# Optimization experiments

Hardware: AMD Instinct MI355X
Metric: run time of the kernel (lower is better)

## Reference

```python
import jax, jax.numpy as jnp
import numpy as np

N = 1 << 20          # ray samples
POS_DIM = 32         # levels * feature_dim (hash_encoding is identity stub)
DENSITY_W = 64
COLOR_W = 64


def sh4_encoding(d):
    # Fourth-order (degree-4, 16-component) real spherical harmonics, vectorized.
    x, y, z = d[..., 0], d[..., 1], d[..., 2]
    xx, yy, zz = x * x, y * y, z * z
    c0 = jnp.full_like(x, 0.28209479177387814)
    comps = [
        c0,
        0.4886025119029199 * y,
        0.4886025119029199 * z,
        0.4886025119029199 * x,
        1.0925484305920792 * x * y,
        1.0925484305920792 * y * z,
        0.9461746957575601 * zz - 0.31539156525252,
        1.0925484305920792 * x * z,
        0.5462742152960396 * (xx - yy),
        0.5900435899266435 * y * (3 * xx - yy),
        2.890611442640554 * x * y * z,
        0.4570457994644658 * y * (5 * zz - 1),
        0.3731763325901154 * z * (5 * zz - 3),
        0.4570457994644658 * x * (5 * zz - 1),
        1.445305721320277 * z * (xx - yy),
        0.5900435899266435 * x * (xx - 3 * yy),
    ]
    return jnp.stack(comps, axis=-1)  # [..., 16]


def setup_inputs() -> dict:
    key = jax.random.key(0)
    ks = jax.random.split(key, 8)
    def dense_init(k, fan_in, fan_out):
        # flax default: lecun_normal kernel, zeros bias
        w = jax.random.normal(k, (fan_in, fan_out), dtype=jnp.float32) / np.sqrt(fan_in)
        b = jnp.zeros((fan_out,), dtype=jnp.float32)
        return w, b
    position = jax.random.normal(ks[0], (N, POS_DIM), dtype=jnp.float32)
    direction = jax.random.normal(ks[1], (N, 3), dtype=jnp.float32)
    W1, b1 = dense_init(ks[2], POS_DIM, DENSITY_W)
    W2, b2 = dense_init(ks[3], DENSITY_W, 16)
    W3, b3 = dense_init(ks[4], 16 + 16, COLOR_W)
    W4, b4 = dense_init(ks[5], COLOR_W, COLOR_W)
    W5, b5 = dense_init(ks[6], COLOR_W, 3)
    return {
        "position": position, "direction": direction,
        "W1": W1, "b1": b1, "W2": W2, "b2": b2,
        "W3": W3, "b3": b3, "W4": W4, "b4": b4,
        "W5": W5, "b5": b5,
    }


def reference(position, direction, W1, b1, W2, b2, W3, b3, W4, b4, W5, b5):
    # Density MLP
    h = jax.nn.relu(position @ W1 + b1)        # [N, 64]
    density = h @ W2 + b2                      # [N, 16]
    # Color MLP on concat(density_feat, SH(dir))
    enc_dir = sh4_encoding(direction)          # [N, 16]
    c = jnp.concatenate([density, enc_dir], axis=-1)  # [N, 32]
    c = jax.nn.relu(c @ W3 + b3)               # [N, 64]
    c = jax.nn.relu(c @ W4 + b4)               # [N, 64]
    c = c @ W5 + b5                            # [N, 3]
    color = jax.nn.sigmoid(c)                  # high_dynamic_range=False
    return (density, color)
```

## Files before the change

### kernel.cpp

```cpp
#include <hip/hip_runtime.h>
#include <hip/hip_bf16.h>

typedef __bf16 bf16_t;
typedef __bf16 bf16x8 __attribute__((ext_vector_type(8)));
typedef float  f32x4  __attribute__((ext_vector_type(4)));

#define TPW   8
#define WAVES 4
#define ROWS_PER_BLOCK (WAVES * TPW * 16)
#define HS 68
#define CS 36

#define FENCE() __asm__ volatile("" ::: "memory")

__device__ __forceinline__ bf16x8 ldrow8(const float* base, size_t elem_off) {
    const float* p = base + elem_off;
    f32x4 a = *(const f32x4*)p;
    f32x4 b = *(const f32x4*)(p + 4);
    bf16x8 r;
    #pragma unroll
    for (int j = 0; j < 4; ++j) { r[j] = (bf16_t)a[j]; r[j+4] = (bf16_t)b[j]; }
    return r;
}

__global__ __launch_bounds__(256) void nerf_fused(
    const float* __restrict__ pos, const float* __restrict__ dir,
    const float* __restrict__ W1, const float* __restrict__ b1,
    const float* __restrict__ W2, const float* __restrict__ b2,
    const float* __restrict__ W3, const float* __restrict__ b3,
    const float* __restrict__ W4, const float* __restrict__ b4,
    const float* __restrict__ W5, const float* __restrict__ b5,
    float* __restrict__ outD, float* __restrict__ outC)
{
    __shared__ float hbuf[WAVES][16 * HS];
    __shared__ float cbuf[WAVES][16 * CS];

    const int tid  = threadIdx.x;
    const int w    = tid >> 6;
    const int lane = tid & 63;
    const int q    = lane >> 4;
    const int n    = lane & 15;

    float* hb = hbuf[w];
    float* cb = cbuf[w];

    bf16x8 w1f[4], w2f[2], w3f[4], w4f[2][4], w5f[2];
    #pragma unroll
    for (int t = 0; t < 4; ++t)
        #pragma unroll
        for (int j = 0; j < 8; ++j)
            w1f[t][j] = (bf16_t)W1[(8*q + j) * 64 + 16*t + n];
    #pragma unroll
    for (int kt = 0; kt < 2; ++kt)
        #pragma unroll
        for (int j = 0; j < 8; ++j)
            w2f[kt][j] = (bf16_t)W2[(32*kt + 8*q + j) * 16 + n];
    #pragma unroll
    for (int t = 0; t < 4; ++t)
        #pragma unroll
        for (int j = 0; j < 8; ++j)
            w3f[t][j] = (bf16_t)W3[(8*q + j) * 64 + 16*t + n];
    #pragma unroll
    for (int kt = 0; kt < 2; ++kt)
        #pragma unroll
        for (int t = 0; t < 4; ++t)
            #pragma unroll
            for (int j = 0; j < 8; ++j)
                w4f[kt][t][j] = (bf16_t)W4[(32*kt + 8*q + j) * 64 + 16*t + n];
    #pragma unroll
    for (int kt = 0; kt < 2; ++kt)
        #pragma unroll
        for (int j = 0; j < 8; ++j)
            w5f[kt][j] = (n < 3) ? (bf16_t)W5[(32*kt + 8*q + j) * 3 + n]
                                 : (bf16_t)0.0f;
    float b1f[4], b3f[4], b4f[4];
    #pragma unroll
    for (int t = 0; t < 4; ++t) {
        b1f[t] = b1[16*t + n];
        b3f[t] = b3[16*t + n];
        b4f[t] = b4[16*t + n];
    }
    const float b2f = b2[n];
    const float b5f = (n < 3) ? b5[n] : 0.0f;

    const f32x4 zero4 = {0.f, 0.f, 0.f, 0.f};

    const int waveRow0 = blockIdx.x * ROWS_PER_BLOCK + w * (TPW * 16);

    bf16x8 pfrag = ldrow8(pos, (size_t)(waveRow0 + n) * 32 + 8*q);

    for (int t = 0; t < TPW; ++t) {
        const int row0 = waveRow0 + t * 16;
        const int tn   = (t + 1 < TPW) ? t + 1 : t;
        bf16x8 pnext = ldrow8(pos, (size_t)(waveRow0 + tn*16 + n) * 32 + 8*q);

        f32x4 acc1[4];
        #pragma unroll
        for (int tt = 0; tt < 4; ++tt)
            acc1[tt] = __builtin_amdgcn_mfma_f32_16x16x32_bf16(pfrag, w1f[tt], zero4, 0, 0, 0);
        #pragma unroll
        for (int r = 0; r < 4; ++r) {
            float* p = hb + (4*q + r) * HS + n;
            p[0]  = fmaxf(acc1[0][r] + b1f[0], 0.f);
            p[16] = fmaxf(acc1[1][r] + b1f[1], 0.f);
            p[32] = fmaxf(acc1[2][r] + b1f[2], 0.f);
            p[48] = fmaxf(acc1[3][r] + b1f[3], 0.f);
        }
        FENCE();
        bf16x8 a2[2];
        #pragma unroll
        for (int kt = 0; kt < 2; ++kt) {
            const f32x4* pr = (const f32x4*)(hb + n * HS + 32*kt + 8*q);
            f32x4 u0 = pr[0], u1 = pr[1];
            #pragma unroll
            for (int j = 0; j < 4; ++j) { a2[kt][j] = (bf16_t)u0[j]; a2[kt][4+j] = (bf16_t)u1[j]; }
        }

        f32x4 acc2 = __builtin_amdgcn_mfma_f32_16x16x32_bf16(a2[0], w2f[0], zero4, 0, 0, 0);
        acc2 = __builtin_amdgcn_mfma_f32_16x16x32_bf16(a2[1], w2f[1], acc2, 0, 0, 0);
        {
            float* p = cb + (4*q) * CS + n;
            p[0]    = acc2[0] + b2f;
            p[CS]   = acc2[1] + b2f;
            p[2*CS] = acc2[2] + b2f;
            p[3*CS] = acc2[3] + b2f;
        }
        FENCE();

        {
            const int rr = lane >> 2;
            const int cg = lane & 3;
            f32x4 dv = *(const f32x4*)(cb + rr * CS + 4*cg);
            *(f32x4*)(outD + (size_t)(row0 + rr) * 16 + 4*cg) = dv;
        }

        float av[8];
        {
            const f32x4* pr = (const f32x4*)(cb + n * CS + 8*(q & 1));
            f32x4 u0 = pr[0], u1 = pr[1];
            #pragma unroll
            for (int j = 0; j < 4; ++j) { av[j] = u0[j]; av[4+j] = u1[j]; }
        }
        if (q >= 2) {
            const size_t db = (size_t)(row0 + n) * 3;
            const float x = dir[db + 0], y = dir[db + 1], z = dir[db + 2];
            const float xx = x*x, yy = y*y, zz = z*z;
            if (q == 2) {
                av[0] = 0.28209479177387814f;
                av[1] = 0.4886025119029199f * y;
                av[2] = 0.4886025119029199f * z;
                av[3] = 0.4886025119029199f * x;
                av[4] = 1.0925484305920792f * x * y;
                av[5] = 1.0925484305920792f * y * z;
                av[6] = 0.9461746957575601f * zz - 0.31539156525252f;
                av[7] = 1.0925484305920792f * x * z;
            } else {
                av[0] = 0.5462742152960396f * (xx - yy);
                av[1] = 0.5900435899266435f * y * (3.f*xx - yy);
                av[2] = 2.890611442640554f * x * y * z;
                av[3] = 0.4570457994644658f * y * (5.f*zz - 1.f);
                av[4] = 0.3731763325901154f * z * (5.f*zz - 3.f);
                av[5] = 0.4570457994644658f * x * (5.f*zz - 1.f);
                av[6] = 1.445305721320277f  * z * (xx - yy);
                av[7] = 0.5900435899266435f * x * (xx - 3.f*yy);
            }
        }
        bf16x8 a3;
        #pragma unroll
        for (int j = 0; j < 8; ++j) a3[j] = (bf16_t)av[j];

        f32x4 acc3[4];
        #pragma unroll
        for (int tt = 0; tt < 4; ++tt)
            acc3[tt] = __builtin_amdgcn_mfma_f32_16x16x32_bf16(a3, w3f[tt], zero4, 0, 0, 0);
        FENCE();
        #pragma unroll
        for (int r = 0; r < 4; ++r) {
            float* p = hb + (4*q + r) * HS + n;
            p[0]  = fmaxf(acc3[0][r] + b3f[0], 0.f);
            p[16] = fmaxf(acc3[1][r] + b3f[1], 0.f);
            p[32] = fmaxf(acc3[2][r] + b3f[2], 0.f);
            p[48] = fmaxf(acc3[3][r] + b3f[3], 0.f);
        }
        FENCE();
        bf16x8 a4[2];
        #pragma unroll
        for (int kt = 0; kt < 2; ++kt) {
            const f32x4* pr = (const f32x4*)(hb + n * HS + 32*kt + 8*q);
            f32x4 u0 = pr[0], u1 = pr[1];
            #pragma unroll
            for (int j = 0; j < 4; ++j) { a4[kt][j] = (bf16_t)u0[j]; a4[kt][4+j] = (bf16_t)u1[j]; }
        }

        f32x4 acc4[4];
        #pragma unroll
        for (int tt = 0; tt < 4; ++tt) {
            acc4[tt] = __builtin_amdgcn_mfma_f32_16x16x32_bf16(a4[0], w4f[0][tt], zero4, 0, 0, 0);
            acc4[tt] = __builtin_amdgcn_mfma_f32_16x16x32_bf16(a4[1], w4f[1][tt], acc4[tt], 0, 0, 0);
        }
        FENCE();
        #pragma unroll
        for (int r = 0; r < 4; ++r) {
            float* p = hb + (4*q + r) * HS + n;
            p[0]  = fmaxf(acc4[0][r] + b4f[0], 0.f);
            p[16] = fmaxf(acc4[1][r] + b4f[1], 0.f);
            p[32] = fmaxf(acc4[2][r] + b4f[2], 0.f);
            p[48] = fmaxf(acc4[3][r] + b4f[3], 0.f);
        }
        FENCE();
        bf16x8 a5[2];
        #pragma unroll
        for (int kt = 0; kt < 2; ++kt) {
            const f32x4* pr = (const f32x4*)(hb + n * HS + 32*kt + 8*q);
            f32x4 u0 = pr[0], u1 = pr[1];
            #pragma unroll
            for (int j = 0; j < 4; ++j) { a5[kt][j] = (bf16_t)u0[j]; a5[kt][4+j] = (bf16_t)u1[j]; }
        }

        f32x4 acc5 = __builtin_amdgcn_mfma_f32_16x16x32_bf16(a5[0], w5f[0], zero4, 0, 0, 0);
        acc5 = __builtin_amdgcn_mfma_f32_16x16x32_bf16(a5[1], w5f[1], acc5, 0, 0, 0);
        if (n < 3) {
            float* p = cb + (4*q) * CS + 32 + n;
            #pragma unroll
            for (int r = 0; r < 4; ++r) {
                float v = acc5[r] + b5f;
                p[r*CS] = 1.f / (1.f + __expf(-v));
            }
        }
        FENCE();
        if (lane < 48) {
            const int s = lane / 3, c = lane - 3*s;
            outC[(size_t)(row0 + s) * 3 + c] = cb[s * CS + 32 + c];
        }
        FENCE();

        pfrag = pnext;
    }
}

extern "C" void kernel_launch(void* const* d_in, const int* in_sizes, int n_in,
                              void* d_out, int out_size, void* d_ws, size_t ws_size,
                              hipStream_t stream) {
    const float* pos = (const float*)d_in[0];
    const float* dir = (const float*)d_in[1];
    const float* W1  = (const float*)d_in[2];
    const float* b1  = (const float*)d_in[3];
    const float* W2  = (const float*)d_in[4];
    const float* b2  = (const float*)d_in[5];
    const float* W3  = (const float*)d_in[6];
    const float* b3  = (const float*)d_in[7];
    const float* W4  = (const float*)d_in[8];
    const float* b4  = (const float*)d_in[9];
    const float* W5  = (const float*)d_in[10];
    const float* b5  = (const float*)d_in[11];

    const int N = in_sizes[0] / 32;
    float* outD = (float*)d_out;
    float* outC = outD + (size_t)N * 16;

    const int grid = N / ROWS_PER_BLOCK;
    nerf_fused<<<grid, WAVES * 64, 0, stream>>>(pos, dir, W1, b1, W2, b2, W3, b3,
                                                W4, b4, W5, b5, outD, outC);
}
```

Measured before the change: 283.7 us.

## Chain MLP layers in registers via transposed 16x16x16 MFMA, drop LDS hidden buffers

```diff
diff --git a/kernel.cpp b/kernel.cpp
--- a/kernel.cpp
+++ b/kernel.cpp
@@ -2,26 +2,29 @@
 #include <hip/hip_bf16.h>
 
 typedef __bf16 bf16_t;
-typedef __bf16 bf16x8 __attribute__((ext_vector_type(8)));
-typedef float  f32x4  __attribute__((ext_vector_type(4)));
+typedef short  s4    __attribute__((ext_vector_type(4)));
+typedef float  f32x4 __attribute__((ext_vector_type(4)));
 
 #define TPW   8
 #define WAVES 4
 #define ROWS_PER_BLOCK (WAVES * TPW * 16)
-#define HS 68
 #define CS 36
 
 #define FENCE() __asm__ volatile("" ::: "memory")
 
-__device__ __forceinline__ bf16x8 ldrow8(const float* base, size_t elem_off) {
-    const float* p = base + elem_off;
-    f32x4 a = *(const f32x4*)p;
-    f32x4 b = *(const f32x4*)(p + 4);
-    bf16x8 r;
-    #pragma unroll
-    for (int j = 0; j < 4; ++j) { r[j] = (bf16_t)a[j]; r[j+4] = (bf16_t)b[j]; }
+__device__ __forceinline__ short bfs(float f) {
+    return __builtin_bit_cast(short, (bf16_t)f);
+}
+__device__ __forceinline__ s4 pack4(f32x4 a) {
+    s4 r; r[0]=bfs(a[0]); r[1]=bfs(a[1]); r[2]=bfs(a[2]); r[3]=bfs(a[3]); return r;
+}
+__device__ __forceinline__ s4 relu_pack4(f32x4 a) {
+    s4 r;
+    r[0]=bfs(fmaxf(a[0],0.f)); r[1]=bfs(fmaxf(a[1],0.f));
+    r[2]=bfs(fmaxf(a[2],0.f)); r[3]=bfs(fmaxf(a[3],0.f));
     return r;
 }
+#define MFMA16(a,b,c) __builtin_amdgcn_mfma_f32_16x16x16bf16_1k(a, b, c, 0, 0, 0)
 
 __global__ __launch_bounds__(256) void nerf_fused(
     const float* __restrict__ pos, const float* __restrict__ dir,
@@ -32,7 +35,6 @@
     const float* __restrict__ W5, const float* __restrict__ b5,
     float* __restrict__ outD, float* __restrict__ outC)
 {
-    __shared__ float hbuf[WAVES][16 * HS];
     __shared__ float cbuf[WAVES][16 * CS];
 
     const int tid  = threadIdx.x;
@@ -41,92 +43,90 @@
     const int q    = lane >> 4;
     const int n    = lane & 15;
 
-    float* hb = hbuf[w];
     float* cb = cbuf[w];
 
-    bf16x8 w1f[4], w2f[2], w3f[4], w4f[2][4], w5f[2];
-    #pragma unroll
-    for (int t = 0; t < 4; ++t)
-        #pragma unroll
-        for (int j = 0; j < 8; ++j)
-            w1f[t][j] = (bf16_t)W1[(8*q + j) * 64 + 16*t + n];
-    #pragma unroll
-    for (int kt = 0; kt < 2; ++kt)
-        #pragma unroll
-        for (int j = 0; j < 8; ++j)
-            w2f[kt][j] = (bf16_t)W2[(32*kt + 8*q + j) * 16 + n];
-    #pragma unroll
-    for (int t = 0; t < 4; ++t)
-        #pragma unroll
-        for (int j = 0; j < 8; ++j)
-            w3f[t][j] = (bf16_t)W3[(8*q + j) * 64 + 16*t + n];
-    #pragma unroll
-    for (int kt = 0; kt < 2; ++kt)
-        #pragma unroll
-        for (int t = 0; t < 4; ++t)
-            #pragma unroll
-            for (int j = 0; j < 8; ++j)
-                w4f[kt][t][j] = (bf16_t)W4[(32*kt + 8*q + j) * 64 + 16*t + n];
-    #pragma unroll
-    for (int kt = 0; kt < 2; ++kt)
-        #pragma unroll
-        for (int j = 0; j < 8; ++j)
-            w5f[kt][j] = (n < 3) ? (bf16_t)W5[(32*kt + 8*q + j) * 3 + n]
-                                 : (bf16_t)0.0f;
-    float b1f[4], b3f[4], b4f[4];
-    #pragma unroll
-    for (int t = 0; t < 4; ++t) {
-        b1f[t] = b1[16*t + n];
-        b3f[t] = b3[16*t + n];
-        b4f[t] = b4[16*t + n];
+    s4 wa1[4][2], wa2[4], wa3[4][2], wa4[4][4], wa5[4];
+    #pragma unroll
+    for (int t = 0; t < 4; ++t)
+        #pragma unroll
+        for (int kt = 0; kt < 2; ++kt)
+            #pragma unroll
+            for (int i = 0; i < 4; ++i)
+                wa1[t][kt][i] = bfs(W1[(16*kt + 4*q + i) * 64 + 16*t + n]);
+    #pragma unroll
+    for (int kt = 0; kt < 4; ++kt)
+        #pragma unroll
+        for (int i = 0; i < 4; ++i)
+            wa2[kt][i] = bfs(W2[(16*kt + 4*q + i) * 16 + n]);
+    #pragma unroll
+    for (int t = 0; t < 4; ++t)
+        #pragma unroll
+        for (int kt = 0; kt < 2; ++kt)
+            #pragma unroll
+            for (int i = 0; i < 4; ++i)
+                wa3[t][kt][i] = bfs(W3[(16*kt + 4*q + i) * 64 + 16*t + n]);
+    #pragma unroll
+    for (int t = 0; t < 4; ++t)
+        #pragma unroll
+        for (int kt = 0; kt < 4; ++kt)
+            #pragma unroll
+            for (int i = 0; i < 4; ++i)
+                wa4[t][kt][i] = bfs(W4[(16*kt + 4*q + i) * 64 + 16*t + n]);
+    #pragma unroll
+    for (int kt = 0; kt < 4; ++kt)
+        #pragma unroll
+        for (int i = 0; i < 4; ++i)
+            wa5[kt][i] = (n < 3) ? bfs(W5[(16*kt + 4*q + i) * 3 + n]) : (short)0;
+
+    f32x4 bi1[4], bi3[4], bi4[4], bi2, bi5;
+    #pragma unroll
+    for (int t = 0; t < 4; ++t)
+        #pragma unroll
+        for (int r = 0; r < 4; ++r) {
+            bi1[t][r] = b1[16*t + 4*q + r];
+            bi3[t][r] = b3[16*t + 4*q + r];
+            bi4[t][r] = b4[16*t + 4*q + r];
+        }
+    #pragma unroll
+    for (int r = 0; r < 4; ++r) {
+        bi2[r] = b2[4*q + r];
+        bi5[r] = (q == 0 && r < 3) ? b5[r] : 0.f;
     }
-    const float b2f = b2[n];
-    const float b5f = (n < 3) ? b5[n] : 0.0f;
-
-    const f32x4 zero4 = {0.f, 0.f, 0.f, 0.f};
 
     const int waveRow0 = blockIdx.x * ROWS_PER_BLOCK + w * (TPW * 16);
 
-    bf16x8 pfrag = ldrow8(pos, (size_t)(waveRow0 + n) * 32 + 8*q);
+    f32x4 pa = *(const f32x4*)(pos + (size_t)(waveRow0 + n) * 32 + 4*q);
+    f32x4 pb = *(const f32x4*)(pos + (size_t)(waveRow0 + n) * 32 + 16 + 4*q);
+    float dx = dir[(size_t)(waveRow0 + n) * 3 + 0];
+    float dy = dir[(size_t)(waveRow0 + n) * 3 + 1];
+    float dz = dir[(size_t)(waveRow0 + n) * 3 + 2];
 
     for (int t = 0; t < TPW; ++t) {
         const int row0 = waveRow0 + t * 16;
-        const int tn   = (t + 1 < TPW) ? t + 1 : t;
-        bf16x8 pnext = ldrow8(pos, (size_t)(waveRow0 + tn*16 + n) * 32 + 8*q);
-
-        f32x4 acc1[4];
-        #pragma unroll
-        for (int tt = 0; tt < 4; ++tt)
-            acc1[tt] = __builtin_amdgcn_mfma_f32_16x16x32_bf16(pfrag, w1f[tt], zero4, 0, 0, 0);
-        #pragma unroll
-        for (int r = 0; r < 4; ++r) {
-            float* p = hb + (4*q + r) * HS + n;
-            p[0]  = fmaxf(acc1[0][r] + b1f[0], 0.f);
-            p[16] = fmaxf(acc1[1][r] + b1f[1], 0.f);
-            p[32] = fmaxf(acc1[2][r] + b1f[2], 0.f);
-            p[48] = fmaxf(acc1[3][r] + b1f[3], 0.f);
-        }
+        const int rn   = waveRow0 + ((t + 1 < TPW) ? t + 1 : t) * 16;
+        f32x4 pa2 = *(const f32x4*)(pos + (size_t)(rn + n) * 32 + 4*q);
+        f32x4 pb2 = *(const f32x4*)(pos + (size_t)(rn + n) * 32 + 16 + 4*q);
+        float dx2 = dir[(size_t)(rn + n) * 3 + 0];
+        float dy2 = dir[(size_t)(rn + n) * 3 + 1];
+        float dz2 = dir[(size_t)(rn + n) * 3 + 2];
+
+        s4 xb0 = pack4(pa), xb1 = pack4(pb);
+
+        s4 hf[4];
+        #pragma unroll
+        for (int tt = 0; tt < 4; ++tt) {
+            f32x4 h = MFMA16(wa1[tt][0], xb0, bi1[tt]);
+            h = MFMA16(wa1[tt][1], xb1, h);
+            hf[tt] = relu_pack4(h);
+        }
+
+        f32x4 d2 = bi2;
+        #pragma unroll
+        for (int kt = 0; kt < 4; ++kt)
+            d2 = MFMA16(wa2[kt], hf[kt], d2);
+
+        *(f32x4*)(cb + n * CS + 4*q) = d2;
         FENCE();
-        bf16x8 a2[2];
-        #pragma unroll
-        for (int kt = 0; kt < 2; ++kt) {
-            const f32x4* pr = (const f32x4*)(hb + n * HS + 32*kt + 8*q);
-            f32x4 u0 = pr[0], u1 = pr[1];
-            #pragma unroll
-            for (int j = 0; j < 4; ++j) { a2[kt][j] = (bf16_t)u0[j]; a2[kt][4+j] = (bf16_t)u1[j]; }
-        }
-
-        f32x4 acc2 = __builtin_amdgcn_mfma_f32_16x16x32_bf16(a2[0], w2f[0], zero4, 0, 0, 0);
-        acc2 = __builtin_amdgcn_mfma_f32_16x16x32_bf16(a2[1], w2f[1], acc2, 0, 0, 0);
-        {
-            float* p = cb + (4*q) * CS + n;
-            p[0]    = acc2[0] + b2f;
-            p[CS]   = acc2[1] + b2f;
-            p[2*CS] = acc2[2] + b2f;
-            p[3*CS] = acc2[3] + b2f;
-        }
-        FENCE();
-
         {
             const int rr = lane >> 2;
             const int cg = lane & 3;
@@ -134,98 +134,63 @@
             *(f32x4*)(outD + (size_t)(row0 + rr) * 16 + 4*cg) = dv;
         }
 
-        float av[8];
+        s4 cf0 = pack4(d2);
+        f32x4 shv;
         {
-            const f32x4* pr = (const f32x4*)(cb + n * CS + 8*(q & 1));
-            f32x4 u0 = pr[0], u1 = pr[1];
-            #pragma unroll
-            for (int j = 0; j < 4; ++j) { av[j] = u0[j]; av[4+j] = u1[j]; }
-        }
-        if (q >= 2) {
-            const size_t db = (size_t)(row0 + n) * 3;
-            const float x = dir[db + 0], y = dir[db + 1], z = dir[db + 2];
-            const float xx = x*x, yy = y*y, zz = z*z;
-            if (q == 2) {
-                av[0] = 0.28209479177387814f;
-                av[1] = 0.4886025119029199f * y;
-                av[2] = 0.4886025119029199f * z;
-                av[3] = 0.4886025119029199f * x;
-                av[4] = 1.0925484305920792f * x * y;
-                av[5] = 1.0925484305920792f * y * z;
-                av[6] = 0.9461746957575601f * zz - 0.31539156525252f;
-                av[7] = 1.0925484305920792f * x * z;
+            const float xx = dx*dx, yy = dy*dy, zz = dz*dz;
+            if (q == 0) {
+                shv[0] = 0.28209479177387814f;
+                shv[1] = 0.4886025119029199f * dy;
+                shv[2] = 0.4886025119029199f * dz;
+                shv[3] = 0.4886025119029199f * dx;
+            } else if (q == 1) {
+                shv[0] = 1.0925484305920792f * dx * dy;
+                shv[1] = 1.0925484305920792f * dy * dz;
+                shv[2] = 0.9461746957575601f * zz - 0.31539156525252f;
+                shv[3] = 1.0925484305920792f * dx * dz;
+            } else if (q == 2) {
+                shv[0] = 0.5462742152960396f * (xx - yy);
+                shv[1] = 0.5900435899266435f * dy * (3.f*xx - yy);
+                shv[2] = 2.890611442640554f * dx * dy * dz;
+                shv[3] = 0.4570457994644658f * dy * (5.f*zz - 1.f);
             } else {
-                av[0] = 0.5462742152960396f * (xx - yy);
-                av[1] = 0.5900435899266435f * y * (3.f*xx - yy);
-                av[2] = 2.890611442640554f * x * y * z;
-                av[3] = 0.4570457994644658f * y * (5.f*zz - 1.f);
-                av[4] = 0.3731763325901154f * z * (5.f*zz - 3.f);
-                av[5] = 0.4570457994644658f * x * (5.f*zz - 1.f);
-                av[6] = 1.445305721320277f  * z * (xx - yy);
-                av[7] = 0.5900435899266435f * x * (xx - 3.f*yy);
+                shv[0] = 0.3731763325901154f * dz * (5.f*zz - 3.f);
+                shv[1] = 0.4570457994644658f * dx * (5.f*zz - 1.f);
+                shv[2] = 1.445305721320277f  * dz * (xx - yy);
+                shv[3] = 0.5900435899266435f * dx * (xx - 3.f*yy);
             }
         }
-        bf16x8 a3;
-        #pragma unroll
-        for (int j = 0; j < 8; ++j) a3[j] = (bf16_t)av[j];
-
-        f32x4 acc3[4];
-        #pragma unroll
-        for (int tt = 0; tt < 4; ++tt)
-            acc3[tt] = __builtin_amdgcn_mfma_f32_16x16x32_bf16(a3, w3f[tt], zero4, 0, 0, 0);
-        FENCE();
-        #pragma unroll
-        for (int r = 0; r < 4; ++r) {
-            float* p = hb + (4*q + r) * HS + n;
-            p[0]  = fmaxf(acc3[0][r] + b3f[0], 0.f);
-            p[16] = fmaxf(acc3[1][r] + b3f[1], 0.f);
-            p[32] = fmaxf(acc3[2][r] + b3f[2], 0.f);
-            p[48] = fmaxf(acc3[3][r] + b3f[3], 0.f);
-        }
-        FENCE();
-        bf16x8 a4[2];
-        #pragma unroll
-        for (int kt = 0; kt < 2; ++kt) {
-            const f32x4* pr = (const f32x4*)(hb + n * HS + 32*kt + 8*q);
-            f32x4 u0 = pr[0], u1 = pr[1];
-            #pragma unroll
-            for (int j = 0; j < 4; ++j) { a4[kt][j] = (bf16_t)u0[j]; a4[kt][4+j] = (bf16_t)u1[j]; }
-        }
-
-        f32x4 acc4[4];
+        s4 cf1 = pack4(shv);
+
+        s4 gf[4];
         #pragma unroll
         for (int tt = 0; tt < 4; ++tt) {
-            acc4[tt] = __builtin_amdgcn_mfma_f32_16x16x32_bf16(a4[0], w4f[0][tt], zero4, 0, 0, 0);
-            acc4[tt] = __builtin_amdgcn_mfma_f32_16x16x32_bf16(a4[1], w4f[1][tt], acc4[tt], 0, 0, 0);
-        }
-        FENCE();
-        #pragma unroll
-        for (int r = 0; r < 4; ++r) {
-            float* p = hb + (4*q + r) * HS + n;
-            p[0]  = fmaxf(acc4[0][r] + b4f[0], 0.f);
-            p[16] = fmaxf(acc4[1][r] + b4f[1], 0.f);
-            p[32] = fmaxf(acc4[2][r] + b4f[2], 0.f);
-            p[48] = fmaxf(acc4[3][r] + b4f[3], 0.f);
-        }
-        FENCE();
-        bf16x8 a5[2];
-        #pragma unroll
-        for (int kt = 0; kt < 2; ++kt) {
-            const f32x4* pr = (const f32x4*)(hb + n * HS + 32*kt + 8*q);
-            f32x4 u0 = pr[0], u1 = pr[1];
-            #pragma unroll
-            for (int j = 0; j < 4; ++j) { a5[kt][j] = (bf16_t)u0[j]; a5[kt][4+j] = (bf16_t)u1[j]; }
-        }
-
-        f32x4 acc5 = __builtin_amdgcn_mfma_f32_16x16x32_bf16(a5[0], w5f[0], zero4, 0, 0, 0);
-        acc5 = __builtin_amdgcn_mfma_f32_16x16x32_bf16(a5[1], w5f[1], acc5, 0, 0, 0);
-        if (n < 3) {
-            float* p = cb + (4*q) * CS + 32 + n;
-            #pragma unroll
-            for (int r = 0; r < 4; ++r) {
-                float v = acc5[r] + b5f;
-                p[r*CS] = 1.f / (1.f + __expf(-v));
-            }
+            f32x4 g = MFMA16(wa3[tt][0], cf0, bi3[tt]);
+            g = MFMA16(wa3[tt][1], cf1, g);
+            gf[tt] = relu_pack4(g);
+        }
+
+        s4 ef[4];
+        #pragma unroll
+        for (int tt = 0; tt < 4; ++tt) {
+            f32x4 e = bi4[tt];
+            #pragma unroll
+            for (int kt = 0; kt < 4; ++kt)
+                e = MFMA16(wa4[tt][kt], gf[kt], e);
+            ef[tt] = relu_pack4(e);
+        }
+
+        f32x4 c5 = bi5;
+        #pragma unroll
+        for (int kt = 0; kt < 4; ++kt)
+            c5 = MFMA16(wa5[kt], ef[kt], c5);
+        if (q == 0) {
+            f32x4 cv;
+            cv[0] = 1.f / (1.f + __expf(-c5[0]));
+            cv[1] = 1.f / (1.f + __expf(-c5[1]));
+            cv[2] = 1.f / (1.f + __expf(-c5[2]));
+            cv[3] = 0.f;
+            *(f32x4*)(cb + n * CS + 32) = cv;
         }
         FENCE();
         if (lane < 48) {
@@ -234,7 +199,7 @@
         }
         FENCE();
 
-        pfrag = pnext;
+        pa = pa2; pb = pb2; dx = dx2; dy = dy2; dz = dz2;
     }
 }
 
```

After: 277.4 us. 2.2% less time.
